# Performance work log

Hardware: AMD Instinct MI355X
Metric: run time of the kernel (lower is better)

The kernel has to match this reference:

```python
import jax, jax.numpy as jnp
import numpy as np

B, N, L = 16, 512, 512          # batch, compound atoms, protein words
DIM = 10                         # compound feature dim
DM, H, DK, DFF = 128, 8, 16, 512 # transformer dims
LG, LO = 3, 3                    # layer_gnn, layer_output
NFP, NW = 10000, 10000           # vocab sizes
NEG = -9e15                      # GAT mask sentinel (matches torch code)


def _layernorm(x, g, b, eps=1e-6):
    # annotated-transformer LayerNorm: unbiased std, eps added to std
    m = jnp.mean(x, -1, keepdims=True)
    s = jnp.std(x, -1, keepdims=True, ddof=1)
    return g * (x - m) / (s + eps) + b


def _pos_encoding(length, d_model):
    pos = np.arange(length)[:, None]
    div = np.exp(np.arange(0, d_model, 2) * (-np.log(10000.0) / d_model))
    pe = np.zeros((length, d_model), np.float32)
    pe[:, 0::2] = np.sin(pos * div)
    pe[:, 1::2] = np.cos(pos * div)
    return jnp.asarray(pe)


def setup_inputs():
    ks = iter(jax.random.split(jax.random.key(0), 64))
    def nrm(shape, scale):
        return jax.random.normal(next(ks), shape, jnp.float32) * scale
    return dict(
        fingerprints=jax.random.randint(next(ks), (B, N), 0, NFP, jnp.int32),
        fp_mask=jnp.ones((B, N), jnp.float32),
        adjacency=jax.random.randint(next(ks), (B, N, N), 0, 2, jnp.int32),
        words=jax.random.randint(next(ks), (B, L), 0, NW, jnp.int32),
        words_mask=jnp.ones((B, L), jnp.float32),
        emb_fp=nrm((NFP, DIM), 0.1),
        emb_word=nrm((NW, DM), 0.1),
        Wg=nrm((LG, DIM, DIM), 0.3), bg=jnp.zeros((LG, DIM), jnp.float32),
        attn_a=nrm((LG, 2 * DIM), 0.3),
        Wq=nrm((DM, DM), 0.09), bq=jnp.zeros((DM,), jnp.float32),
        Wk=nrm((DM, DM), 0.09), bk=jnp.zeros((DM,), jnp.float32),
        Wv=nrm((DM, DM), 0.09), bv=jnp.zeros((DM,), jnp.float32),
        Wo=nrm((DM, DM), 0.09), bo=jnp.zeros((DM,), jnp.float32),
        ln1_g=jnp.ones((DM,), jnp.float32), ln1_b=jnp.zeros((DM,), jnp.float32),
        ln2_g=jnp.ones((DM,), jnp.float32), ln2_b=jnp.zeros((DM,), jnp.float32),
        lnf_g=jnp.ones((DM,), jnp.float32), lnf_b=jnp.zeros((DM,), jnp.float32),
        W1=nrm((DM, DFF), 0.09), b1=jnp.zeros((DFF,), jnp.float32),
        W2=nrm((DFF, DM), 0.045), b2=jnp.zeros((DM,), jnp.float32),
        Wtout=nrm((DM, DIM), 0.09), btout=jnp.zeros((DIM,), jnp.float32),
        Watt=nrm((DIM, DIM), 0.3), batt=jnp.zeros((DIM,), jnp.float32),
        Wout=nrm((LO, 2 * DIM, 2 * DIM), 0.2), bout=jnp.zeros((LO, 2 * DIM), jnp.float32),
        Wint=nrm((2 * DIM, 2), 0.2), bint=jnp.zeros((2,), jnp.float32),
    )


def _forward(fingerprints, fp_mask, adjacency, words, words_mask,
             emb_fp, emb_word, Wg, bg, attn_a,
             Wq, bq, Wk, bk, Wv, bv, Wo, bo,
             ln1_g, ln1_b, ln2_g, ln2_b, lnf_g, lnf_b,
             W1, b1, W2, b2, Wtout, btout,
             Watt, batt, Wout, bout, Wint, bint):
    # ---- GAT over compound graph (dropout disabled = eval/deterministic) ----
    xs = emb_fp[fingerprints]                     # [B,N,DIM]
    mask = fp_mask[:, :, None]                    # [B,N,1]
    adj = adjacency > 0
    for i in range(LG):
        h = jax.nn.relu(xs @ Wg[i] + bg[i]) * mask
        # e[b,i,j] = leaky_relu(a1.h_i + a2.h_j)  == leaky_relu([h_i||h_j] @ a)
        s1 = h @ attn_a[i, :DIM]                  # [B,N]
        s2 = h @ attn_a[i, DIM:]                  # [B,N]
        e = jax.nn.leaky_relu(s1[:, :, None] + s2[:, None, :])  # [B,N,N]
        att = jax.nn.softmax(jnp.where(adj, e, NEG), axis=2)
        xs = xs + att @ h
    compound = jnp.mean(xs * mask, axis=1, keepdims=True)       # [B,1,DIM]

    # ---- transformer encoder, 1 layer, annotated-transformer (pre-norm) ----
    x = emb_word[words] * jnp.sqrt(jnp.float32(DM)) + _pos_encoding(L, DM)
    m4 = words_mask[:, None, None, :] > 0         # [B,1,1,L]
    xn = _layernorm(x, ln1_g, ln1_b)
    heads = lambda t: t.reshape(B, L, H, DK).transpose(0, 2, 1, 3)
    q, k, v = heads(xn @ Wq + bq), heads(xn @ Wk + bk), heads(xn @ Wv + bv)
    scores = jnp.einsum('bhqd,bhkd->bhqk', q, k) / jnp.sqrt(jnp.float32(DK))
    p = jax.nn.softmax(jnp.where(m4, scores, -1e9), axis=-1)
    attn = jnp.einsum('bhqk,bhkd->bhqd', p, v).transpose(0, 2, 1, 3).reshape(B, L, DM)
    x = x + (attn @ Wo + bo)
    xn = _layernorm(x, ln2_g, ln2_b)
    x = x + (jax.nn.relu(xn @ W1 + b1) @ W2 + b2)
    x = _layernorm(x, lnf_g, lnf_b)
    word_vectors = jax.nn.relu(x) @ Wtout + btout  # [B,L,DIM]

    # ---- tanh cross-attention (attention_cnn) ----
    hc = jax.nn.relu(compound @ Watt + batt)       # [B,1,DIM]
    hp = jax.nn.relu(word_vectors @ Watt + batt)   # [B,L,DIM]
    w = jnp.tanh(jnp.einsum('bxd,bld->bxl', hc, hp))  # [B,1,L]
    protein = jnp.mean(w.transpose(0, 2, 1) * hp, axis=1, keepdims=True)  # [B,1,DIM]

    cat = jnp.concatenate([compound, protein], axis=2)  # [B,1,2*DIM]
    for j in range(LO):
        cat = jax.nn.relu(cat @ Wout[j] + bout[j])
    return jnp.squeeze(cat @ Wint + bint, axis=1)        # [B,2]


def reference(fingerprints, fp_mask, adjacency, words, words_mask,
              emb_fp, emb_word, Wg, bg, attn_a,
              Wq, bq, Wk, bk, Wv, bv, Wo, bo,
              ln1_g, ln1_b, ln2_g, ln2_b, lnf_g, lnf_b,
              W1, b1, W2, b2, Wtout, btout,
              Watt, batt, Wout, bout, Wint, bint):
    return _forward(fingerprints, fp_mask, adjacency, words, words_mask,
                    emb_fp, emb_word, Wg, bg, attn_a,
                    Wq, bq, Wk, bk, Wv, bv, Wo, bo,
                    ln1_g, ln1_b, ln2_g, ln2_b, lnf_g, lnf_b,
                    W1, b1, W2, b2, Wtout, btout,
                    Watt, batt, Wout, bout, Wint, bint)
```

## Files before the change

### kernel.cpp

```cpp
#include <hip/hip_runtime.h>
#include <hip/hip_bf16.h>
#include <math.h>

#define B 16
#define N 512
#define L 512
#define DIM 10
#define DM 128
#define H 8
#define DK 16
#define DFF 512
#define LG 3
#define LO 3
#define NEGV -9.0e15f
#define RF 16
#define AQR 64

__device__ __forceinline__ float wave_reduce_sum(float v) {
    #pragma unroll
    for (int o = 32; o > 0; o >>= 1) v += __shfl_down(v, o, 64);
    return v;
}


__global__ void k_embed_fp(const int* __restrict__ fing, const float* __restrict__ emb_fp,
                           float* __restrict__ xs) {
    int idx = blockIdx.x * blockDim.x + threadIdx.x;
    if (idx >= B * N * DIM) return;
    int d = idx % DIM;
    int bn = idx / DIM;
    xs[idx] = emb_fp[fing[bn] * DIM + d];
}

__global__ void k_gnn_h(const float* __restrict__ xs, const float* __restrict__ fp_mask,
                        const float* __restrict__ Wg, const float* __restrict__ bg,
                        const float* __restrict__ aatt,
                        float* __restrict__ h, float* __restrict__ s1, float* __restrict__ s2) {
    int bn = blockIdx.x * blockDim.x + threadIdx.x;
    if (bn >= B * N) return;
    float x[DIM];
    #pragma unroll
    for (int d = 0; d < DIM; d++) x[d] = xs[bn * DIM + d];
    float m = fp_mask[bn];
    float a1 = 0.f, a2 = 0.f;
    #pragma unroll
    for (int j = 0; j < DIM; j++) {
        float acc = bg[j];
        #pragma unroll
        for (int d = 0; d < DIM; d++) acc += x[d] * Wg[d * DIM + j];
        acc = fmaxf(acc, 0.f) * m;
        h[bn * DIM + j] = acc;
        a1 += acc * aatt[j];
        a2 += acc * aatt[DIM + j];
    }
    s1[bn] = a1;
    s2[bn] = a2;
}

__global__ void k_gnn_att(const float* __restrict__ h, const float* __restrict__ s1,
                          const float* __restrict__ s2, const int* __restrict__ adj,
                          float* __restrict__ xs) {
    int b  = blockIdx.x / (N / 16);
    int rg = blockIdx.x % (N / 16);
    int t = threadIdx.x;
    int g  = t >> 4;
    int ll = t & 15;
    int i = rg * 16 + g;

    __shared__ float h_s[N * DIM];
    __shared__ float s2_s[N];

    const float* hb = h + (long)b * N * DIM;
    for (int idx = t; idx < N * DIM; idx += 256) h_s[idx] = hb[idx];
    for (int j = t; j < N; j += 256) s2_s[j] = s2[b * N + j];
    __syncthreads();

    float s1v = s1[b * N + i];
    const int* adjrow = adj + ((long)b * N + i) * N;

    float e[32];
    #pragma unroll
    for (int c = 0; c < 32; c++) {
        int j = c * 16 + ll;
        float xsc = s1v + s2_s[j];
        xsc = xsc > 0.f ? xsc : 0.01f * xsc;
        e[c] = (adjrow[j] > 0) ? xsc : NEGV;
    }
    float m = e[0];
    #pragma unroll
    for (int c = 1; c < 32; c++) m = fmaxf(m, e[c]);
    #pragma unroll
    for (int off = 1; off < 16; off <<= 1) m = fmaxf(m, __shfl_xor(m, off, 64));

    float sum = 0.f;
    float a[DIM];
    #pragma unroll
    for (int d = 0; d < DIM; d++) a[d] = 0.f;
    #pragma unroll
    for (int c = 0; c < 32; c++) {
        float p = expf(e[c] - m);
        sum += p;
        int j = c * 16 + ll;
        #pragma unroll
        for (int d = 0; d < DIM; d++) a[d] += p * h_s[j * DIM + d];
    }
    #pragma unroll
    for (int off = 1; off < 16; off <<= 1) {
        sum += __shfl_xor(sum, off, 64);
        #pragma unroll
        for (int d = 0; d < DIM; d++) a[d] += __shfl_xor(a[d], off, 64);
    }
    if (ll < DIM) {
        float av = a[0];
        if (ll == 1) av = a[1]; else if (ll == 2) av = a[2]; else if (ll == 3) av = a[3];
        else if (ll == 4) av = a[4]; else if (ll == 5) av = a[5]; else if (ll == 6) av = a[6];
        else if (ll == 7) av = a[7]; else if (ll == 8) av = a[8]; else if (ll == 9) av = a[9];
        xs[((long)b * N + i) * DIM + ll] += av / sum;
    }
}

__global__ void k_compound(const float* __restrict__ xs, const float* __restrict__ fp_mask,
                           const float* __restrict__ Watt, const float* __restrict__ batt,
                           float* __restrict__ compound, float* __restrict__ hc) {
    int b = blockIdx.x;
    int t = threadIdx.x;
    int wid = t >> 6, lane = t & 63;
    float lacc[DIM];
    #pragma unroll
    for (int d = 0; d < DIM; d++) lacc[d] = 0.f;
    for (int n = t; n < N; n += 256) {
        float m = fp_mask[b * N + n];
        #pragma unroll
        for (int d = 0; d < DIM; d++) lacc[d] += xs[((long)b * N + n) * DIM + d] * m;
    }
    __shared__ float red[4][DIM];
    __shared__ float comp_s[DIM];
    #pragma unroll
    for (int d = 0; d < DIM; d++) lacc[d] = wave_reduce_sum(lacc[d]);
    if (lane == 0) {
        #pragma unroll
        for (int d = 0; d < DIM; d++) red[wid][d] = lacc[d];
    }
    __syncthreads();
    if (t < DIM) {
        float c = (red[0][t] + red[1][t] + red[2][t] + red[3][t]) / (float)N;
        compound[b * DIM + t] = c;
        comp_s[t] = c;
    }
    __syncthreads();
    if (t < DIM) {
        float acc = batt[t];
        #pragma unroll
        for (int e = 0; e < DIM; e++) acc += comp_s[e] * Watt[e * DIM + t];
        hc[b * DIM + t] = fmaxf(acc, 0.f);
    }
}


__global__ void k_pe(float* __restrict__ pe) {
    int idx = blockIdx.x * blockDim.x + threadIdx.x;
    if (idx >= L * DM) return;
    int d = idx % DM, l = idx / DM;
    int k = d >> 1;
    double div = exp((double)(2 * k) * (-log(10000.0) / (double)DM));
    double ang = (double)l * div;
    pe[idx] = (d & 1) ? (float)cos(ang) : (float)sin(ang);
}

__global__ void k_embed_word(const int* __restrict__ words, const float* __restrict__ emb,
                             const float* __restrict__ pe, float* __restrict__ x) {
    long idx = (long)blockIdx.x * blockDim.x + threadIdx.x;
    if (idx >= (long)B * L * DM) return;
    int d = idx % DM;
    long bl = idx / DM;
    int l = (int)(bl % L);
    x[idx] = emb[(long)words[bl] * DM + d] * sqrtf(128.0f) + pe[l * DM + d];
}

__global__ void k_layernorm(const float* __restrict__ x, const float* __restrict__ g,
                            const float* __restrict__ bb, float* __restrict__ out) {
    int row = blockIdx.x;
    int t = threadIdx.x;
    int wid = t >> 6, lane = t & 63;
    float v = x[(long)row * DM + t];
    float s = wave_reduce_sum(v);
    __shared__ float r2[2], r3[2];
    if (lane == 0) r2[wid] = s;
    __syncthreads();
    float mean = (r2[0] + r2[1]) / (float)DM;
    float dv = v - mean;
    float q = wave_reduce_sum(dv * dv);
    if (lane == 0) r3[wid] = q;
    __syncthreads();
    float sd = sqrtf((r3[0] + r3[1]) / (float)(DM - 1)) + 1e-6f;
    out[(long)row * DM + t] = g[t] * dv / sd + bb[t];
}

__global__ void k_qkv(const float* __restrict__ xn,
                      const float* __restrict__ Wq, const float* __restrict__ bq,
                      const float* __restrict__ Wk, const float* __restrict__ bk,
                      const float* __restrict__ Wv, const float* __restrict__ bv,
                      float* __restrict__ q, float* __restrict__ k, float* __restrict__ v) {
    long row0 = (long)blockIdx.x * RF;
    int t = threadIdx.x;
    __shared__ float xs_s[RF * DM];
    for (int i = t; i < RF * DM; i += 384) xs_s[i] = xn[row0 * DM + i];
    __syncthreads();
    int proj = t / DM;
    int j = t % DM;
    const float* W    = proj == 0 ? Wq : (proj == 1 ? Wk : Wv);
    const float* bias = proj == 0 ? bq : (proj == 1 ? bk : bv);
    float* out        = proj == 0 ? q  : (proj == 1 ? k  : v);
    float acc[RF];
    #pragma unroll
    for (int r = 0; r < RF; r++) acc[r] = bias[j];
    for (int d = 0; d < DM; d++) {
        float w = W[d * DM + j];
        #pragma unroll
        for (int r = 0; r < RF; r++) acc[r] += xs_s[r * DM + d] * w;
    }
    #pragma unroll
    for (int r = 0; r < RF; r++) {
        long row = row0 + r;
        int b = (int)(row / L), l = (int)(row % L);
        out[(((long)b * H + j / DK) * L + l) * DK + (j % DK)] = acc[r];
    }
}

__global__ void k_attn(const float* __restrict__ q, const float* __restrict__ k,
                       const float* __restrict__ v, const float* __restrict__ wmask,
                       float* __restrict__ attnout) {
    int blk = blockIdx.x;
    int qc = blk % (L / AQR);
    int bh = blk / (L / AQR);
    int b = bh / H, hh = bh % H;
    int t = threadIdx.x;
    int sl = t & 3;
    int r = t >> 2;
    int l = qc * AQR + r;

    __shared__ float4 k_s[L * 4];
    __shared__ float wm_s[L];
    const float4* kb4 = (const float4*)(k + (long)bh * L * DK);
    for (int i = t; i < L * 4; i += 256) k_s[i] = kb4[i];
    for (int j = t; j < L; j += 256) wm_s[j] = wmask[b * L + j];
    __syncthreads();

    float4 qr = ((const float4*)(q + ((long)bh * L + l) * DK))[sl];
    qr.x *= 0.25f; qr.y *= 0.25f; qr.z *= 0.25f; qr.w *= 0.25f;

    const float4* vb4 = (const float4*)(v + (long)bh * L * DK);

    float m = -1e30f, ssum = 0.f;
    float4 acc = make_float4(0.f, 0.f, 0.f, 0.f);

    for (int c = 0; c < L / 8; c++) {
        int j0 = c * 8;
        float s8[8];
        #pragma unroll
        for (int jj = 0; jj < 8; jj++) {
            float4 kk = k_s[(j0 + jj) * 4 + sl];
            s8[jj] = qr.x * kk.x + qr.y * kk.y + qr.z * kk.z + qr.w * kk.w;
        }
        #pragma unroll
        for (int jj = 0; jj < 8; jj++) {
            s8[jj] += __shfl_xor(s8[jj], 1, 64);
            s8[jj] += __shfl_xor(s8[jj], 2, 64);
            s8[jj] = (wm_s[j0 + jj] > 0.f) ? s8[jj] : -1e9f;
        }
        float cm = fmaxf(fmaxf(fmaxf(s8[0], s8[1]), fmaxf(s8[2], s8[3])),
                         fmaxf(fmaxf(s8[4], s8[5]), fmaxf(s8[6], s8[7])));
        float mn = fmaxf(m, cm);
        float scale = __expf(m - mn);
        ssum *= scale;
        acc.x *= scale; acc.y *= scale; acc.z *= scale; acc.w *= scale;
        #pragma unroll
        for (int jj = 0; jj < 8; jj++) {
            float p = __expf(s8[jj] - mn);
            ssum += p;
            float4 vv = vb4[(j0 + jj) * 4 + sl];
            acc.x += p * vv.x; acc.y += p * vv.y; acc.z += p * vv.z; acc.w += p * vv.w;
        }
        m = mn;
    }

    float inv = 1.f / ssum;
    float4* outp = (float4*)(attnout + ((long)b * L + l) * DM + hh * DK);
    outp[sl] = make_float4(acc.x * inv, acc.y * inv, acc.z * inv, acc.w * inv);
}

__global__ void k_oproj(const float* __restrict__ attnout, const float* __restrict__ Wo,
                        const float* __restrict__ bo, float* __restrict__ x) {
    long row0 = (long)blockIdx.x * RF;
    int t = threadIdx.x;
    __shared__ float a_s[RF * DM];
    for (int i = t; i < RF * DM; i += 128) a_s[i] = attnout[row0 * DM + i];
    __syncthreads();
    float acc[RF];
    #pragma unroll
    for (int r = 0; r < RF; r++) acc[r] = bo[t];
    for (int d = 0; d < DM; d++) {
        float w = Wo[d * DM + t];
        #pragma unroll
        for (int r = 0; r < RF; r++) acc[r] += a_s[r * DM + d] * w;
    }
    #pragma unroll
    for (int r = 0; r < RF; r++) x[(row0 + r) * DM + t] += acc[r];
}

__global__ void k_ffn(const float* __restrict__ xn, const float* __restrict__ W1,
                      const float* __restrict__ b1, const float* __restrict__ W2,
                      const float* __restrict__ b2, float* __restrict__ x) {
    long row0 = (long)blockIdx.x * RF;
    int t = threadIdx.x;
    __shared__ float xs_s[RF * DM];
    __shared__ float h_s[RF * DFF];
    for (int i = t; i < RF * DM; i += 512) xs_s[i] = xn[row0 * DM + i];
    __syncthreads();
    {
        float acc[RF];
        #pragma unroll
        for (int r = 0; r < RF; r++) acc[r] = b1[t];
        for (int d = 0; d < DM; d++) {
            float w = W1[d * DFF + t];
            #pragma unroll
            for (int r = 0; r < RF; r++) acc[r] += xs_s[r * DM + d] * w;
        }
        #pragma unroll
        for (int r = 0; r < RF; r++) h_s[r * DFF + t] = fmaxf(acc[r], 0.f);
    }
    __syncthreads();
    int col = t & 127, rq = t >> 7;
    float acc2[4];
    #pragma unroll
    for (int rr = 0; rr < 4; rr++) acc2[rr] = b2[col];
    for (int f = 0; f < DFF; f++) {
        float w = W2[f * DM + col];
        #pragma unroll
        for (int rr = 0; rr < 4; rr++) acc2[rr] += h_s[(rq * 4 + rr) * DFF + f] * w;
    }
    #pragma unroll
    for (int rr = 0; rr < 4; rr++) x[(row0 + rq * 4 + rr) * DM + col] += acc2[rr];
}

__global__ void k_lnf_hp(const float* __restrict__ x, const float* __restrict__ g,
                         const float* __restrict__ bb, const float* __restrict__ Wtout,
                         const float* __restrict__ btout, const float* __restrict__ Watt,
                         const float* __restrict__ batt, float* __restrict__ hp) {
    int row = blockIdx.x;
    int t = threadIdx.x;
    int wid = t >> 6, lane = t & 63;
    float v = x[(long)row * DM + t];
    float s = wave_reduce_sum(v);
    __shared__ float r2[2], r3[2];
    if (lane == 0) r2[wid] = s;
    __syncthreads();
    float mean = (r2[0] + r2[1]) / (float)DM;
    float dv = v - mean;
    float qq = wave_reduce_sum(dv * dv);
    if (lane == 0) r3[wid] = qq;
    __syncthreads();
    float sd = sqrtf((r3[0] + r3[1]) / (float)(DM - 1)) + 1e-6f;
    float xnv = g[t] * dv / sd + bb[t];
    __shared__ float rrelu[DM];
    rrelu[t] = fmaxf(xnv, 0.f);
    __syncthreads();
    __shared__ float wv_s[DIM];
    if (t < DIM) {
        float acc = btout[t];
        for (int d = 0; d < DM; d++) acc += rrelu[d] * Wtout[d * DIM + t];
        wv_s[t] = acc;
    }
    __syncthreads();
    if (t < DIM) {
        float acc = batt[t];
        #pragma unroll
        for (int e = 0; e < DIM; e++) acc += wv_s[e] * Watt[e * DIM + t];
        hp[(long)row * DIM + t] = fmaxf(acc, 0.f);
    }
}

__global__ void k_final(const float* __restrict__ hp, const float* __restrict__ hc,
                        const float* __restrict__ compound, const float* __restrict__ Wout,
                        const float* __restrict__ bout, const float* __restrict__ Wint,
                        const float* __restrict__ bint, float* __restrict__ out) {
    int b = blockIdx.x;
    int t = threadIdx.x;
    int wid = t >> 6, lane = t & 63;

    __shared__ float wout_s[LO * 2 * DIM * 2 * DIM];
    __shared__ float bout_s[LO * 2 * DIM];
    __shared__ float wint_s[2 * DIM * 2];
    __shared__ float bint_s[2];
    __shared__ float hc_s[DIM];
    __shared__ float red[4][DIM];
    __shared__ float cat_s[2 * DIM];
    __shared__ float tmp_s[2 * DIM];

    for (int i = t; i < LO * 2 * DIM * 2 * DIM; i += 256) wout_s[i] = Wout[i];
    for (int i = t; i < LO * 2 * DIM; i += 256) bout_s[i] = bout[i];
    for (int i = t; i < 2 * DIM * 2; i += 256) wint_s[i] = Wint[i];
    if (t < 2) bint_s[t] = bint[t];
    if (t < DIM) hc_s[t] = hc[b * DIM + t];
    __syncthreads();

    float lacc[DIM];
    #pragma unroll
    for (int e = 0; e < DIM; e++) lacc[e] = 0.f;
    for (int l = t; l < L; l += 256) {
        const float* hpl = hp + ((long)b * L + l) * DIM;
        float hv[DIM];
        float dot = 0.f;
        #pragma unroll
        for (int e = 0; e < DIM; e++) { hv[e] = hpl[e]; dot += hc_s[e] * hv[e]; }
        float w = tanhf(dot);
        #pragma unroll
        for (int e = 0; e < DIM; e++) lacc[e] += w * hv[e];
    }
    #pragma unroll
    for (int e = 0; e < DIM; e++) lacc[e] = wave_reduce_sum(lacc[e]);
    if (lane == 0) {
        #pragma unroll
        for (int e = 0; e < DIM; e++) red[wid][e] = lacc[e];
    }
    __syncthreads();
    if (t < DIM) {
        cat_s[t] = compound[b * DIM + t];
        cat_s[DIM + t] = (red[0][t] + red[1][t] + red[2][t] + red[3][t]) / (float)L;
    }
    __syncthreads();

    for (int j = 0; j < LO; j++) {
        float acc = 0.f;
        if (t < 2 * DIM) {
            acc = bout_s[j * 2 * DIM + t];
            #pragma unroll
            for (int e = 0; e < 2 * DIM; e++)
                acc += cat_s[e] * wout_s[j * 2 * DIM * 2 * DIM + e * 2 * DIM + t];
            acc = fmaxf(acc, 0.f);
            tmp_s[t] = acc;
        }
        __syncthreads();
        if (t < 2 * DIM) cat_s[t] = tmp_s[t];
        __syncthreads();
    }
    if (t < 2) {
        float o = bint_s[t];
        #pragma unroll
        for (int e = 0; e < 2 * DIM; e++) o += cat_s[e] * wint_s[e * 2 + t];
        out[b * 2 + t] = o;
    }
}

extern "C" void kernel_launch(void* const* d_in, const int* in_sizes, int n_in,
                              void* d_out, int out_size, void* d_ws, size_t ws_size,
                              hipStream_t stream) {
    (void)in_sizes; (void)n_in; (void)out_size; (void)ws_size;
    const int*   fingerprints = (const int*)d_in[0];
    const float* fp_mask      = (const float*)d_in[1];
    const int*   adjacency    = (const int*)d_in[2];
    const int*   words        = (const int*)d_in[3];
    const float* words_mask   = (const float*)d_in[4];
    const float* emb_fp       = (const float*)d_in[5];
    const float* emb_word     = (const float*)d_in[6];
    const float* Wg   = (const float*)d_in[7];
    const float* bg   = (const float*)d_in[8];
    const float* attn_a = (const float*)d_in[9];
    const float* Wq = (const float*)d_in[10];
    const float* bq = (const float*)d_in[11];
    const float* Wk = (const float*)d_in[12];
    const float* bk = (const float*)d_in[13];
    const float* Wv = (const float*)d_in[14];
    const float* bv = (const float*)d_in[15];
    const float* Wo = (const float*)d_in[16];
    const float* bo = (const float*)d_in[17];
    const float* ln1_g = (const float*)d_in[18];
    const float* ln1_b = (const float*)d_in[19];
    const float* ln2_g = (const float*)d_in[20];
    const float* ln2_b = (const float*)d_in[21];
    const float* lnf_g = (const float*)d_in[22];
    const float* lnf_b = (const float*)d_in[23];
    const float* W1 = (const float*)d_in[24];
    const float* b1 = (const float*)d_in[25];
    const float* W2 = (const float*)d_in[26];
    const float* b2 = (const float*)d_in[27];
    const float* Wtout = (const float*)d_in[28];
    const float* btout = (const float*)d_in[29];
    const float* Watt  = (const float*)d_in[30];
    const float* batt  = (const float*)d_in[31];
    const float* Wout  = (const float*)d_in[32];
    const float* bout  = (const float*)d_in[33];
    const float* Wint  = (const float*)d_in[34];
    const float* bint  = (const float*)d_in[35];
    float* out = (float*)d_out;

    float* w = (float*)d_ws;
    float* xs = w;        w += B * N * DIM;
    float* h  = w;        w += B * N * DIM;
    float* s1 = w;        w += B * N;
    float* s2 = w;        w += B * N;
    float* compound = w;  w += B * DIM;
    float* hc = w;        w += B * DIM;
    float* pe = w;        w += L * DM;
    float* x  = w;        w += (long)B * L * DM;
    float* xn = w;        w += (long)B * L * DM;
    float* qb = w;        w += (long)B * H * L * DK;
    float* kb = w;        w += (long)B * H * L * DK;
    float* vb = w;        w += (long)B * H * L * DK;
    float* attnout = w;   w += (long)B * L * DM;
    float* hp = w;        w += (long)B * L * DIM;

    k_embed_fp<<<(B * N * DIM + 255) / 256, 256, 0, stream>>>(fingerprints, emb_fp, xs);
    for (int i = 0; i < LG; i++) {
        k_gnn_h<<<(B * N + 255) / 256, 256, 0, stream>>>(
            xs, fp_mask, Wg + i * DIM * DIM, bg + i * DIM, attn_a + i * 2 * DIM, h, s1, s2);
        k_gnn_att<<<B * (N / 16), 256, 0, stream>>>(h, s1, s2, adjacency, xs);
    }
    k_compound<<<B, 256, 0, stream>>>(xs, fp_mask, Watt, batt, compound, hc);

    k_pe<<<(L * DM + 255) / 256, 256, 0, stream>>>(pe);
    k_embed_word<<<(B * L * DM + 255) / 256, 256, 0, stream>>>(words, emb_word, pe, x);
    k_layernorm<<<B * L, DM, 0, stream>>>(x, ln1_g, ln1_b, xn);
    k_qkv<<<B * L / RF, 3 * DM, 0, stream>>>(xn, Wq, bq, Wk, bk, Wv, bv, qb, kb, vb);
    k_attn<<<B * H * (L / AQR), 256, 0, stream>>>(qb, kb, vb, words_mask, attnout);
    k_oproj<<<B * L / RF, DM, 0, stream>>>(attnout, Wo, bo, x);
    k_layernorm<<<B * L, DM, 0, stream>>>(x, ln2_g, ln2_b, xn);
    k_ffn<<<B * L / RF, DFF, 0, stream>>>(xn, W1, b1, W2, b2, x);
    k_lnf_hp<<<B * L, DM, 0, stream>>>(x, lnf_g, lnf_b, Wtout, btout, Watt, batt, hp);
    k_final<<<B, 256, 0, stream>>>(hp, hc, compound, Wout, bout, Wint, bint, out);
}
```

Measured before the change: 277.1 us.

## Restructure attention kernel into split-key flash attention with two queries per thread

Each thread now computes two query rows across the full 16-dim head over one eighth of the key range, instead of four threads sharing a row's dimensions and scanning all keys. K, V and the mask are read directly from global memory rather than staged in shared memory, and the eight partial softmax states are merged with xor shuffles at the end. This removes the per-score cross-lane reductions and the shared-memory staging barrier, and reuses each K/V load across two queries. In exchange it uses many more registers, reads K/V through the cache instead of LDS, and adds a log-step merge epilogue.

```diff
diff --git a/kernel.cpp b/kernel.cpp
--- a/kernel.cpp
+++ b/kernel.cpp
@@ -235,58 +235,122 @@
     int bh = blk / (L / AQR);
     int b = bh / H, hh = bh % H;
     int t = threadIdx.x;
-    int sl = t & 3;
-    int r = t >> 2;
-    int l = qc * AQR + r;
-
-    __shared__ float4 k_s[L * 4];
-    __shared__ float wm_s[L];
+    int seg = t & 7;
+    int pr = t >> 3;
+    int l0 = qc * AQR + pr * 2;
+
+    const float4* qp = (const float4*)(q + ((long)bh * L + l0) * DK);
+    float4 qa0 = qp[0], qa1 = qp[1], qa2 = qp[2], qa3 = qp[3];
+    float4 qb0 = qp[4], qb1 = qp[5], qb2 = qp[6], qb3 = qp[7];
+    qa0.x*=0.25f;qa0.y*=0.25f;qa0.z*=0.25f;qa0.w*=0.25f;
+    qa1.x*=0.25f;qa1.y*=0.25f;qa1.z*=0.25f;qa1.w*=0.25f;
+    qa2.x*=0.25f;qa2.y*=0.25f;qa2.z*=0.25f;qa2.w*=0.25f;
+    qa3.x*=0.25f;qa3.y*=0.25f;qa3.z*=0.25f;qa3.w*=0.25f;
+    qb0.x*=0.25f;qb0.y*=0.25f;qb0.z*=0.25f;qb0.w*=0.25f;
+    qb1.x*=0.25f;qb1.y*=0.25f;qb1.z*=0.25f;qb1.w*=0.25f;
+    qb2.x*=0.25f;qb2.y*=0.25f;qb2.z*=0.25f;qb2.w*=0.25f;
+    qb3.x*=0.25f;qb3.y*=0.25f;qb3.z*=0.25f;qb3.w*=0.25f;
+
     const float4* kb4 = (const float4*)(k + (long)bh * L * DK);
-    for (int i = t; i < L * 4; i += 256) k_s[i] = kb4[i];
-    for (int j = t; j < L; j += 256) wm_s[j] = wmask[b * L + j];
-    __syncthreads();
-
-    float4 qr = ((const float4*)(q + ((long)bh * L + l) * DK))[sl];
-    qr.x *= 0.25f; qr.y *= 0.25f; qr.z *= 0.25f; qr.w *= 0.25f;
-
     const float4* vb4 = (const float4*)(v + (long)bh * L * DK);
-
-    float m = -1e30f, ssum = 0.f;
-    float4 acc = make_float4(0.f, 0.f, 0.f, 0.f);
-
-    for (int c = 0; c < L / 8; c++) {
-        int j0 = c * 8;
-        float s8[8];
+    const float4* wm4 = (const float4*)(wmask + (long)b * L);
+
+    float m0 = -1e30f, m1 = -1e30f, ss0 = 0.f, ss1 = 0.f;
+    float4 a00 = make_float4(0,0,0,0), a01 = a00, a02 = a00, a03 = a00;
+    float4 a10 = a00, a11 = a00, a12 = a00, a13 = a00;
+
+    for (int c = 0; c < 8; c++) {
+        int j0 = seg * 64 + c * 8;
+        float s0[8], s1[8];
         #pragma unroll
         for (int jj = 0; jj < 8; jj++) {
-            float4 kk = k_s[(j0 + jj) * 4 + sl];
-            s8[jj] = qr.x * kk.x + qr.y * kk.y + qr.z * kk.z + qr.w * kk.w;
+            const float4* kp = kb4 + (long)(j0 + jj) * 4;
+            float4 k0 = kp[0], k1 = kp[1], k2 = kp[2], k3 = kp[3];
+            s0[jj] = qa0.x*k0.x + qa0.y*k0.y + qa0.z*k0.z + qa0.w*k0.w
+                   + qa1.x*k1.x + qa1.y*k1.y + qa1.z*k1.z + qa1.w*k1.w
+                   + qa2.x*k2.x + qa2.y*k2.y + qa2.z*k2.z + qa2.w*k2.w
+                   + qa3.x*k3.x + qa3.y*k3.y + qa3.z*k3.z + qa3.w*k3.w;
+            s1[jj] = qb0.x*k0.x + qb0.y*k0.y + qb0.z*k0.z + qb0.w*k0.w
+                   + qb1.x*k1.x + qb1.y*k1.y + qb1.z*k1.z + qb1.w*k1.w
+                   + qb2.x*k2.x + qb2.y*k2.y + qb2.z*k2.z + qb2.w*k2.w
+                   + qb3.x*k3.x + qb3.y*k3.y + qb3.z*k3.z + qb3.w*k3.w;
         }
+        float4 wma = wm4[j0 / 4], wmb = wm4[j0 / 4 + 1];
+        s0[0] = wma.x > 0.f ? s0[0] : -1e9f;  s1[0] = wma.x > 0.f ? s1[0] : -1e9f;
+        s0[1] = wma.y > 0.f ? s0[1] : -1e9f;  s1[1] = wma.y > 0.f ? s1[1] : -1e9f;
+        s0[2] = wma.z > 0.f ? s0[2] : -1e9f;  s1[2] = wma.z > 0.f ? s1[2] : -1e9f;
+        s0[3] = wma.w > 0.f ? s0[3] : -1e9f;  s1[3] = wma.w > 0.f ? s1[3] : -1e9f;
+        s0[4] = wmb.x > 0.f ? s0[4] : -1e9f;  s1[4] = wmb.x > 0.f ? s1[4] : -1e9f;
+        s0[5] = wmb.y > 0.f ? s0[5] : -1e9f;  s1[5] = wmb.y > 0.f ? s1[5] : -1e9f;
+        s0[6] = wmb.z > 0.f ? s0[6] : -1e9f;  s1[6] = wmb.z > 0.f ? s1[6] : -1e9f;
+        s0[7] = wmb.w > 0.f ? s0[7] : -1e9f;  s1[7] = wmb.w > 0.f ? s1[7] : -1e9f;
+
+        float cm0 = fmaxf(fmaxf(fmaxf(s0[0],s0[1]),fmaxf(s0[2],s0[3])),
+                          fmaxf(fmaxf(s0[4],s0[5]),fmaxf(s0[6],s0[7])));
+        float cm1 = fmaxf(fmaxf(fmaxf(s1[0],s1[1]),fmaxf(s1[2],s1[3])),
+                          fmaxf(fmaxf(s1[4],s1[5]),fmaxf(s1[6],s1[7])));
+        float mn0 = fmaxf(m0, cm0), mn1 = fmaxf(m1, cm1);
+        float sc0 = __expf(m0 - mn0), sc1 = __expf(m1 - mn1);
+        ss0 *= sc0; ss1 *= sc1;
+        a00.x*=sc0;a00.y*=sc0;a00.z*=sc0;a00.w*=sc0;
+        a01.x*=sc0;a01.y*=sc0;a01.z*=sc0;a01.w*=sc0;
+        a02.x*=sc0;a02.y*=sc0;a02.z*=sc0;a02.w*=sc0;
+        a03.x*=sc0;a03.y*=sc0;a03.z*=sc0;a03.w*=sc0;
+        a10.x*=sc1;a10.y*=sc1;a10.z*=sc1;a10.w*=sc1;
+        a11.x*=sc1;a11.y*=sc1;a11.z*=sc1;a11.w*=sc1;
+        a12.x*=sc1;a12.y*=sc1;a12.z*=sc1;a12.w*=sc1;
+        a13.x*=sc1;a13.y*=sc1;a13.z*=sc1;a13.w*=sc1;
+        m0 = mn0; m1 = mn1;
+
         #pragma unroll
         for (int jj = 0; jj < 8; jj++) {
-            s8[jj] += __shfl_xor(s8[jj], 1, 64);
-            s8[jj] += __shfl_xor(s8[jj], 2, 64);
-            s8[jj] = (wm_s[j0 + jj] > 0.f) ? s8[jj] : -1e9f;
+            float p0 = __expf(s0[jj] - m0);
+            float p1 = __expf(s1[jj] - m1);
+            ss0 += p0; ss1 += p1;
+            const float4* vp = vb4 + (long)(j0 + jj) * 4;
+            float4 v0 = vp[0], v1 = vp[1], v2 = vp[2], v3 = vp[3];
+            a00.x += p0*v0.x; a00.y += p0*v0.y; a00.z += p0*v0.z; a00.w += p0*v0.w;
+            a01.x += p0*v1.x; a01.y += p0*v1.y; a01.z += p0*v1.z; a01.w += p0*v1.w;
+            a02.x += p0*v2.x; a02.y += p0*v2.y; a02.z += p0*v2.z; a02.w += p0*v2.w;
+            a03.x += p0*v3.x; a03.y += p0*v3.y; a03.z += p0*v3.z; a03.w += p0*v3.w;
+            a10.x += p1*v0.x; a10.y += p1*v0.y; a10.z += p1*v0.z; a10.w += p1*v0.w;
+            a11.x += p1*v1.x; a11.y += p1*v1.y; a11.z += p1*v1.z; a11.w += p1*v1.w;
+            a12.x += p1*v2.x; a12.y += p1*v2.y; a12.z += p1*v2.z; a12.w += p1*v2.w;
+            a13.x += p1*v3.x; a13.y += p1*v3.y; a13.z += p1*v3.z; a13.w += p1*v3.w;
         }
-        float cm = fmaxf(fmaxf(fmaxf(s8[0], s8[1]), fmaxf(s8[2], s8[3])),
-                         fmaxf(fmaxf(s8[4], s8[5]), fmaxf(s8[6], s8[7])));
-        float mn = fmaxf(m, cm);
-        float scale = __expf(m - mn);
-        ssum *= scale;
-        acc.x *= scale; acc.y *= scale; acc.z *= scale; acc.w *= scale;
-        #pragma unroll
-        for (int jj = 0; jj < 8; jj++) {
-            float p = __expf(s8[jj] - mn);
-            ssum += p;
-            float4 vv = vb4[(j0 + jj) * 4 + sl];
-            acc.x += p * vv.x; acc.y += p * vv.y; acc.z += p * vv.z; acc.w += p * vv.w;
-        }
-        m = mn;
-    }
-
-    float inv = 1.f / ssum;
-    float4* outp = (float4*)(attnout + ((long)b * L + l) * DM + hh * DK);
-    outp[sl] = make_float4(acc.x * inv, acc.y * inv, acc.z * inv, acc.w * inv);
+    }
+
+    #pragma unroll
+    for (int off = 1; off <= 4; off <<= 1) {
+        float m0o = __shfl_xor(m0, off, 64), m1o = __shfl_xor(m1, off, 64);
+        float s0o = __shfl_xor(ss0, off, 64), s1o = __shfl_xor(ss1, off, 64);
+        float mn0 = fmaxf(m0, m0o), mn1 = fmaxf(m1, m1o);
+        float ea0 = __expf(m0 - mn0), eb0 = __expf(m0o - mn0);
+        float ea1 = __expf(m1 - mn1), eb1 = __expf(m1o - mn1);
+        ss0 = ss0 * ea0 + s0o * eb0;
+        ss1 = ss1 * ea1 + s1o * eb1;
+        #define MRG0(f) { float o_ = __shfl_xor(f, off, 64); f = f * ea0 + o_ * eb0; }
+        #define MRG1(f) { float o_ = __shfl_xor(f, off, 64); f = f * ea1 + o_ * eb1; }
+        MRG0(a00.x) MRG0(a00.y) MRG0(a00.z) MRG0(a00.w)
+        MRG0(a01.x) MRG0(a01.y) MRG0(a01.z) MRG0(a01.w)
+        MRG0(a02.x) MRG0(a02.y) MRG0(a02.z) MRG0(a02.w)
+        MRG0(a03.x) MRG0(a03.y) MRG0(a03.z) MRG0(a03.w)
+        MRG1(a10.x) MRG1(a10.y) MRG1(a10.z) MRG1(a10.w)
+        MRG1(a11.x) MRG1(a11.y) MRG1(a11.z) MRG1(a11.w)
+        MRG1(a12.x) MRG1(a12.y) MRG1(a12.z) MRG1(a12.w)
+        MRG1(a13.x) MRG1(a13.y) MRG1(a13.z) MRG1(a13.w)
+        #undef MRG0
+        #undef MRG1
+        m0 = mn0; m1 = mn1;
+    }
+
+    int sl = seg & 3, rr = seg >> 2;
+    float inv = 1.f / (rr ? ss1 : ss0);
+    float4 w4;
+    if (rr == 0) w4 = (sl == 0) ? a00 : (sl == 1) ? a01 : (sl == 2) ? a02 : a03;
+    else         w4 = (sl == 0) ? a10 : (sl == 1) ? a11 : (sl == 2) ? a12 : a13;
+    float4* outp = (float4*)(attnout + ((long)b * L + (l0 + rr)) * DM + hh * DK);
+    outp[sl] = make_float4(w4.x * inv, w4.y * inv, w4.z * inv, w4.w * inv);
 }
 
 __global__ void k_oproj(const float* __restrict__ attnout, const float* __restrict__ Wo,
```

Result: slower. 467.6 us (+68.7%).

## Split attention keys across waves with per-lane full-row queries and merge partials

Applied to the files above, without the earlier changes.

The attention kernel now gives each lane a whole query row and splits the key range across the four waves, one quarter each. K and V are read straight from global memory as wave-uniform broadcast loads, which removes the shared-memory K staging and the shuffle reduction over head-dim sub-lanes. The per-wave online-softmax partials are combined through shared memory by wave 0. This increases register use per thread (16-element accumulators) and adds a merge step, and launch bounds are set to keep occupancy.

```diff
diff --git a/kernel.cpp b/kernel.cpp
--- a/kernel.cpp
+++ b/kernel.cpp
@@ -227,66 +227,113 @@
     }
 }
 
-__global__ void k_attn(const float* __restrict__ q, const float* __restrict__ k,
-                       const float* __restrict__ v, const float* __restrict__ wmask,
-                       float* __restrict__ attnout) {
+__global__ void __launch_bounds__(256, 4)
+k_attn(const float* __restrict__ q, const float* __restrict__ k,
+       const float* __restrict__ v, const float* __restrict__ wmask,
+       float* __restrict__ attnout) {
     int blk = blockIdx.x;
     int qc = blk % (L / AQR);
     int bh = blk / (L / AQR);
     int b = bh / H, hh = bh % H;
     int t = threadIdx.x;
-    int sl = t & 3;
-    int r = t >> 2;
-    int l = qc * AQR + r;
-
-    __shared__ float4 k_s[L * 4];
-    __shared__ float wm_s[L];
+    int lane = t & 63;
+    int wv = t >> 6;
+    int l = qc * AQR + lane;
+
+    const float4* qp = (const float4*)(q + ((long)bh * L + l) * DK);
+    float4 q0 = qp[0], q1 = qp[1], q2 = qp[2], q3 = qp[3];
+    q0.x*=0.25f;q0.y*=0.25f;q0.z*=0.25f;q0.w*=0.25f;
+    q1.x*=0.25f;q1.y*=0.25f;q1.z*=0.25f;q1.w*=0.25f;
+    q2.x*=0.25f;q2.y*=0.25f;q2.z*=0.25f;q2.w*=0.25f;
+    q3.x*=0.25f;q3.y*=0.25f;q3.z*=0.25f;q3.w*=0.25f;
+
     const float4* kb4 = (const float4*)(k + (long)bh * L * DK);
-    for (int i = t; i < L * 4; i += 256) k_s[i] = kb4[i];
-    for (int j = t; j < L; j += 256) wm_s[j] = wmask[b * L + j];
-    __syncthreads();
-
-    float4 qr = ((const float4*)(q + ((long)bh * L + l) * DK))[sl];
-    qr.x *= 0.25f; qr.y *= 0.25f; qr.z *= 0.25f; qr.w *= 0.25f;
-
     const float4* vb4 = (const float4*)(v + (long)bh * L * DK);
-
-    float m = -1e30f, ssum = 0.f;
-    float4 acc = make_float4(0.f, 0.f, 0.f, 0.f);
-
-    for (int c = 0; c < L / 8; c++) {
-        int j0 = c * 8;
+    const float4* wm4 = (const float4*)(wmask + (long)b * L);
+
+    float m = -1e30f, ss = 0.f;
+    float4 a0 = make_float4(0,0,0,0), a1 = a0, a2 = a0, a3 = a0;
+
+    for (int c = 0; c < 16; c++) {
+        int j0 = wv * 128 + c * 8;
         float s8[8];
         #pragma unroll
         for (int jj = 0; jj < 8; jj++) {
-            float4 kk = k_s[(j0 + jj) * 4 + sl];
-            s8[jj] = qr.x * kk.x + qr.y * kk.y + qr.z * kk.z + qr.w * kk.w;
+            const float4* kp = kb4 + (long)(j0 + jj) * 4;
+            float4 k0 = kp[0], k1 = kp[1], k2 = kp[2], k3 = kp[3];
+            s8[jj] = q0.x*k0.x + q0.y*k0.y + q0.z*k0.z + q0.w*k0.w
+                   + q1.x*k1.x + q1.y*k1.y + q1.z*k1.z + q1.w*k1.w
+                   + q2.x*k2.x + q2.y*k2.y + q2.z*k2.z + q2.w*k2.w
+                   + q3.x*k3.x + q3.y*k3.y + q3.z*k3.z + q3.w*k3.w;
         }
+        float4 wma = wm4[j0 / 4], wmb = wm4[j0 / 4 + 1];
+        s8[0] = wma.x > 0.f ? s8[0] : -1e9f;
+        s8[1] = wma.y > 0.f ? s8[1] : -1e9f;
+        s8[2] = wma.z > 0.f ? s8[2] : -1e9f;
+        s8[3] = wma.w > 0.f ? s8[3] : -1e9f;
+        s8[4] = wmb.x > 0.f ? s8[4] : -1e9f;
+        s8[5] = wmb.y > 0.f ? s8[5] : -1e9f;
+        s8[6] = wmb.z > 0.f ? s8[6] : -1e9f;
+        s8[7] = wmb.w > 0.f ? s8[7] : -1e9f;
+
+        float cm = fmaxf(fmaxf(fmaxf(s8[0],s8[1]),fmaxf(s8[2],s8[3])),
+                         fmaxf(fmaxf(s8[4],s8[5]),fmaxf(s8[6],s8[7])));
+        float mn = fmaxf(m, cm);
+        float sc = __expf(m - mn);
+        ss *= sc;
+        a0.x*=sc;a0.y*=sc;a0.z*=sc;a0.w*=sc;
+        a1.x*=sc;a1.y*=sc;a1.z*=sc;a1.w*=sc;
+        a2.x*=sc;a2.y*=sc;a2.z*=sc;a2.w*=sc;
+        a3.x*=sc;a3.y*=sc;a3.z*=sc;a3.w*=sc;
+        m = mn;
+
         #pragma unroll
         for (int jj = 0; jj < 8; jj++) {
-            s8[jj] += __shfl_xor(s8[jj], 1, 64);
-            s8[jj] += __shfl_xor(s8[jj], 2, 64);
-            s8[jj] = (wm_s[j0 + jj] > 0.f) ? s8[jj] : -1e9f;
+            float p = __expf(s8[jj] - m);
+            ss += p;
+            const float4* vp = vb4 + (long)(j0 + jj) * 4;
+            float4 v0 = vp[0], v1 = vp[1], v2 = vp[2], v3 = vp[3];
+            a0.x += p*v0.x; a0.y += p*v0.y; a0.z += p*v0.z; a0.w += p*v0.w;
+            a1.x += p*v1.x; a1.y += p*v1.y; a1.z += p*v1.z; a1.w += p*v1.w;
+            a2.x += p*v2.x; a2.y += p*v2.y; a2.z += p*v2.z; a2.w += p*v2.w;
+            a3.x += p*v3.x; a3.y += p*v3.y; a3.z += p*v3.z; a3.w += p*v3.w;
         }
-        float cm = fmaxf(fmaxf(fmaxf(s8[0], s8[1]), fmaxf(s8[2], s8[3])),
-                         fmaxf(fmaxf(s8[4], s8[5]), fmaxf(s8[6], s8[7])));
-        float mn = fmaxf(m, cm);
-        float scale = __expf(m - mn);
-        ssum *= scale;
-        acc.x *= scale; acc.y *= scale; acc.z *= scale; acc.w *= scale;
-        #pragma unroll
-        for (int jj = 0; jj < 8; jj++) {
-            float p = __expf(s8[jj] - mn);
-            ssum += p;
-            float4 vv = vb4[(j0 + jj) * 4 + sl];
-            acc.x += p * vv.x; acc.y += p * vv.y; acc.z += p * vv.z; acc.w += p * vv.w;
+    }
+
+    __shared__ float part[3][AQR][18];
+    if (wv > 0) {
+        float* p_ = &part[wv - 1][lane][0];
+        p_[0] = m;    p_[1] = ss;
+        p_[2] = a0.x; p_[3] = a0.y; p_[4]  = a0.z; p_[5]  = a0.w;
+        p_[6] = a1.x; p_[7] = a1.y; p_[8]  = a1.z; p_[9]  = a1.w;
+        p_[10]= a2.x; p_[11]= a2.y; p_[12] = a2.z; p_[13] = a2.w;
+        p_[14]= a3.x; p_[15]= a3.y; p_[16] = a3.z; p_[17] = a3.w;
+    }
+    __syncthreads();
+    if (wv == 0) {
+        for (int s = 0; s < 3; s++) {
+            const float* p_ = &part[s][lane][0];
+            float m2 = p_[0], ss2 = p_[1];
+            float mn = fmaxf(m, m2);
+            float ea = __expf(m - mn), eb = __expf(m2 - mn);
+            ss = ss * ea + ss2 * eb;
+            a0.x = a0.x*ea + p_[2]*eb;  a0.y = a0.y*ea + p_[3]*eb;
+            a0.z = a0.z*ea + p_[4]*eb;  a0.w = a0.w*ea + p_[5]*eb;
+            a1.x = a1.x*ea + p_[6]*eb;  a1.y = a1.y*ea + p_[7]*eb;
+            a1.z = a1.z*ea + p_[8]*eb;  a1.w = a1.w*ea + p_[9]*eb;
+            a2.x = a2.x*ea + p_[10]*eb; a2.y = a2.y*ea + p_[11]*eb;
+            a2.z = a2.z*ea + p_[12]*eb; a2.w = a2.w*ea + p_[13]*eb;
+            a3.x = a3.x*ea + p_[14]*eb; a3.y = a3.y*ea + p_[15]*eb;
+            a3.z = a3.z*ea + p_[16]*eb; a3.w = a3.w*ea + p_[17]*eb;
+            m = mn;
         }
-        m = mn;
-    }
-
-    float inv = 1.f / ssum;
-    float4* outp = (float4*)(attnout + ((long)b * L + l) * DM + hh * DK);
-    outp[sl] = make_float4(acc.x * inv, acc.y * inv, acc.z * inv, acc.w * inv);
+        float inv = 1.f / ss;
+        float4* outp = (float4*)(attnout + ((long)b * L + l) * DM + hh * DK);
+        outp[0] = make_float4(a0.x*inv, a0.y*inv, a0.z*inv, a0.w*inv);
+        outp[1] = make_float4(a1.x*inv, a1.y*inv, a1.z*inv, a1.w*inv);
+        outp[2] = make_float4(a2.x*inv, a2.y*inv, a2.z*inv, a2.w*inv);
+        outp[3] = make_float4(a3.x*inv, a3.y*inv, a3.z*inv, a3.w*inv);
+    }
 }
 
 __global__ void k_oproj(const float* __restrict__ attnout, const float* __restrict__ Wo,
```

Measured after the change: 305.0 us. 10.1% more time.

## Restructure attention kernel with double-buffered K/V tiles and key-split per thread

Applied to the files above, without the earlier changes.

The attention kernel now streams K, V and the mask through double-buffered 64-key shared-memory tiles, with a swizzled layout to avoid bank conflicts. Previously only K sat in shared memory and V was read directly from global memory. Each thread now computes two query rows over a slice of 8 keys, so every K/V shared load is reused across both rows. The eight key-groups are merged with shuffle reductions at the end. This is meant to cut per-key global V traffic and shuffle overhead, at the cost of more registers and a barrier on every tile.

```diff
diff --git a/kernel.cpp b/kernel.cpp
--- a/kernel.cpp
+++ b/kernel.cpp
@@ -15,11 +15,21 @@
 #define NEGV -9.0e15f
 #define RF 16
 #define AQR 64
+#define KT 64
+#define NT (L / KT)
 
 __device__ __forceinline__ float wave_reduce_sum(float v) {
     #pragma unroll
     for (int o = 32; o > 0; o >>= 1) v += __shfl_down(v, o, 64);
     return v;
+}
+
+__device__ __forceinline__ float dot16(float4 q0, float4 q1, float4 q2, float4 q3,
+                                       float4 k0, float4 k1, float4 k2, float4 k3) {
+    return q0.x*k0.x + q0.y*k0.y + q0.z*k0.z + q0.w*k0.w
+         + q1.x*k1.x + q1.y*k1.y + q1.z*k1.z + q1.w*k1.w
+         + q2.x*k2.x + q2.y*k2.y + q2.z*k2.z + q2.w*k2.w
+         + q3.x*k3.x + q3.y*k3.y + q3.z*k3.z + q3.w*k3.w;
 }
 
 
@@ -227,66 +237,163 @@
     }
 }
 
-__global__ void k_attn(const float* __restrict__ q, const float* __restrict__ k,
-                       const float* __restrict__ v, const float* __restrict__ wmask,
-                       float* __restrict__ attnout) {
+__global__ void __launch_bounds__(256, 4)
+k_attn(const float* __restrict__ q, const float* __restrict__ k,
+       const float* __restrict__ v, const float* __restrict__ wmask,
+       float* __restrict__ attnout) {
     int blk = blockIdx.x;
     int qc = blk % (L / AQR);
     int bh = blk / (L / AQR);
     int b = bh / H, hh = bh % H;
     int t = threadIdx.x;
-    int sl = t & 3;
-    int r = t >> 2;
-    int l = qc * AQR + r;
-
-    __shared__ float4 k_s[L * 4];
-    __shared__ float wm_s[L];
+    int qg = t >> 3;
+    int kg = t & 7;
+
+    __shared__ float kbuf[2][KT][DK];
+    __shared__ float vbuf[2][KT][DK];
+    __shared__ float mbuf[2][KT];
+
     const float4* kb4 = (const float4*)(k + (long)bh * L * DK);
-    for (int i = t; i < L * 4; i += 256) k_s[i] = kb4[i];
-    for (int j = t; j < L; j += 256) wm_s[j] = wmask[b * L + j];
-    __syncthreads();
-
-    float4 qr = ((const float4*)(q + ((long)bh * L + l) * DK))[sl];
-    qr.x *= 0.25f; qr.y *= 0.25f; qr.z *= 0.25f; qr.w *= 0.25f;
-
     const float4* vb4 = (const float4*)(v + (long)bh * L * DK);
-
-    float m = -1e30f, ssum = 0.f;
-    float4 acc = make_float4(0.f, 0.f, 0.f, 0.f);
-
-    for (int c = 0; c < L / 8; c++) {
-        int j0 = c * 8;
-        float s8[8];
-        #pragma unroll
-        for (int jj = 0; jj < 8; jj++) {
-            float4 kk = k_s[(j0 + jj) * 4 + sl];
-            s8[jj] = qr.x * kk.x + qr.y * kk.y + qr.z * kk.z + qr.w * kk.w;
-        }
-        #pragma unroll
-        for (int jj = 0; jj < 8; jj++) {
-            s8[jj] += __shfl_xor(s8[jj], 1, 64);
-            s8[jj] += __shfl_xor(s8[jj], 2, 64);
-            s8[jj] = (wm_s[j0 + jj] > 0.f) ? s8[jj] : -1e9f;
-        }
-        float cm = fmaxf(fmaxf(fmaxf(s8[0], s8[1]), fmaxf(s8[2], s8[3])),
-                         fmaxf(fmaxf(s8[4], s8[5]), fmaxf(s8[6], s8[7])));
-        float mn = fmaxf(m, cm);
-        float scale = __expf(m - mn);
-        ssum *= scale;
-        acc.x *= scale; acc.y *= scale; acc.z *= scale; acc.w *= scale;
-        #pragma unroll
-        for (int jj = 0; jj < 8; jj++) {
-            float p = __expf(s8[jj] - mn);
-            ssum += p;
-            float4 vv = vb4[(j0 + jj) * 4 + sl];
-            acc.x += p * vv.x; acc.y += p * vv.y; acc.z += p * vv.z; acc.w += p * vv.w;
-        }
-        m = mn;
-    }
-
-    float inv = 1.f / ssum;
-    float4* outp = (float4*)(attnout + ((long)b * L + l) * DM + hh * DK);
-    outp[sl] = make_float4(acc.x * inv, acc.y * inv, acc.z * inv, acc.w * inv);
+    const float*  wm  = wmask + (long)b * L;
+
+    int row0 = qc * AQR + 2 * qg;
+    const float4* qp = (const float4*)(q + ((long)bh * L + row0) * DK);
+    float4 qa[4], qb[4];
+    #pragma unroll
+    for (int i = 0; i < 4; i++) {
+        qa[i] = qp[i];     qb[i] = qp[4 + i];
+        qa[i].x *= 0.25f; qa[i].y *= 0.25f; qa[i].z *= 0.25f; qa[i].w *= 0.25f;
+        qb[i].x *= 0.25f; qb[i].y *= 0.25f; qb[i].z *= 0.25f; qb[i].w *= 0.25f;
+    }
+
+    int skey = t >> 2;
+    int spart = t & 3;
+    int sphys = spart ^ ((skey >> 3) & 3);
+
+    {
+        float4 kr = kb4[t];
+        float4 vr = vb4[t];
+        ((float4*)&kbuf[0][skey][0])[sphys] = kr;
+        ((float4*)&vbuf[0][skey][0])[sphys] = vr;
+        if (t < KT) mbuf[0][t] = (wm[t] > 0.f) ? 0.f : -1e9f;
+    }
+    __syncthreads();
+
+    float m0 = -1e30f, m1 = -1e30f, ss0 = 0.f, ss1 = 0.f;
+    float4 o0[4], o1[4];
+    #pragma unroll
+    for (int i = 0; i < 4; i++) {
+        o0[i] = make_float4(0.f, 0.f, 0.f, 0.f);
+        o1[i] = make_float4(0.f, 0.f, 0.f, 0.f);
+    }
+
+    int sw = kg & 3;
+    int cur = 0;
+    for (int tt = 0; tt < NT; tt++) {
+        float4 kr2, vr2;
+        float mr2 = 1.f;
+        if (tt < NT - 1) {
+            long base = (long)(tt + 1) * KT * 4;
+            kr2 = kb4[base + t];
+            vr2 = vb4[base + t];
+            if (t < KT) mr2 = wm[(tt + 1) * KT + t];
+        }
+
+        float s0[8], s1[8];
+        #pragma unroll
+        for (int kk = 0; kk < 8; kk++) {
+            const float4* kp = (const float4*)&kbuf[cur][kg * 8 + kk][0];
+            float4 k0 = kp[0 ^ sw], k1 = kp[1 ^ sw], k2 = kp[2 ^ sw], k3 = kp[3 ^ sw];
+            s0[kk] = dot16(qa[0], qa[1], qa[2], qa[3], k0, k1, k2, k3);
+            s1[kk] = dot16(qb[0], qb[1], qb[2], qb[3], k0, k1, k2, k3);
+        }
+        {
+            const float4* mp = (const float4*)&mbuf[cur][kg * 8];
+            float4 ma = mp[0], mb_ = mp[1];
+            s0[0] += ma.x;  s1[0] += ma.x;   s0[1] += ma.y;  s1[1] += ma.y;
+            s0[2] += ma.z;  s1[2] += ma.z;   s0[3] += ma.w;  s1[3] += ma.w;
+            s0[4] += mb_.x; s1[4] += mb_.x;  s0[5] += mb_.y; s1[5] += mb_.y;
+            s0[6] += mb_.z; s1[6] += mb_.z;  s0[7] += mb_.w; s1[7] += mb_.w;
+        }
+
+        float cm0 = fmaxf(fmaxf(fmaxf(s0[0], s0[1]), fmaxf(s0[2], s0[3])),
+                          fmaxf(fmaxf(s0[4], s0[5]), fmaxf(s0[6], s0[7])));
+        float cm1 = fmaxf(fmaxf(fmaxf(s1[0], s1[1]), fmaxf(s1[2], s1[3])),
+                          fmaxf(fmaxf(s1[4], s1[5]), fmaxf(s1[6], s1[7])));
+        cm0 = fmaxf(cm0, __shfl_xor(cm0, 1, 64));
+        cm0 = fmaxf(cm0, __shfl_xor(cm0, 2, 64));
+        cm0 = fmaxf(cm0, __shfl_xor(cm0, 4, 64));
+        cm1 = fmaxf(cm1, __shfl_xor(cm1, 1, 64));
+        cm1 = fmaxf(cm1, __shfl_xor(cm1, 2, 64));
+        cm1 = fmaxf(cm1, __shfl_xor(cm1, 4, 64));
+
+        float mn0 = fmaxf(m0, cm0), mn1 = fmaxf(m1, cm1);
+        float sc0 = __expf(m0 - mn0), sc1 = __expf(m1 - mn1);
+        m0 = mn0; m1 = mn1;
+
+        float pls0 = 0.f, pls1 = 0.f;
+        #pragma unroll
+        for (int kk = 0; kk < 8; kk++) {
+            s0[kk] = __expf(s0[kk] - mn0); pls0 += s0[kk];
+            s1[kk] = __expf(s1[kk] - mn1); pls1 += s1[kk];
+        }
+        ss0 = ss0 * sc0 + pls0;
+        ss1 = ss1 * sc1 + pls1;
+        #pragma unroll
+        for (int i = 0; i < 4; i++) {
+            o0[i].x *= sc0; o0[i].y *= sc0; o0[i].z *= sc0; o0[i].w *= sc0;
+            o1[i].x *= sc1; o1[i].y *= sc1; o1[i].z *= sc1; o1[i].w *= sc1;
+        }
+
+        #pragma unroll
+        for (int kk = 0; kk < 8; kk++) {
+            const float4* vp = (const float4*)&vbuf[cur][kg * 8 + kk][0];
+            float4 v0 = vp[0 ^ sw], v1 = vp[1 ^ sw], v2 = vp[2 ^ sw], v3 = vp[3 ^ sw];
+            float p0 = s0[kk], p1 = s1[kk];
+            o0[0].x += p0*v0.x; o0[0].y += p0*v0.y; o0[0].z += p0*v0.z; o0[0].w += p0*v0.w;
+            o0[1].x += p0*v1.x; o0[1].y += p0*v1.y; o0[1].z += p0*v1.z; o0[1].w += p0*v1.w;
+            o0[2].x += p0*v2.x; o0[2].y += p0*v2.y; o0[2].z += p0*v2.z; o0[2].w += p0*v2.w;
+            o0[3].x += p0*v3.x; o0[3].y += p0*v3.y; o0[3].z += p0*v3.z; o0[3].w += p0*v3.w;
+            o1[0].x += p1*v0.x; o1[0].y += p1*v0.y; o1[0].z += p1*v0.z; o1[0].w += p1*v0.w;
+            o1[1].x += p1*v1.x; o1[1].y += p1*v1.y; o1[1].z += p1*v1.z; o1[1].w += p1*v1.w;
+            o1[2].x += p1*v2.x; o1[2].y += p1*v2.y; o1[2].z += p1*v2.z; o1[2].w += p1*v2.w;
+            o1[3].x += p1*v3.x; o1[3].y += p1*v3.y; o1[3].z += p1*v3.z; o1[3].w += p1*v3.w;
+        }
+
+        if (tt < NT - 1) {
+            ((float4*)&kbuf[cur ^ 1][skey][0])[sphys] = kr2;
+            ((float4*)&vbuf[cur ^ 1][skey][0])[sphys] = vr2;
+            if (t < KT) mbuf[cur ^ 1][t] = (mr2 > 0.f) ? 0.f : -1e9f;
+        }
+        __syncthreads();
+        cur ^= 1;
+    }
+
+    #pragma unroll
+    for (int off = 1; off <= 4; off <<= 1) {
+        ss0 += __shfl_xor(ss0, off, 64);
+        ss1 += __shfl_xor(ss1, off, 64);
+        #pragma unroll
+        for (int i = 0; i < 4; i++) {
+            o0[i].x += __shfl_xor(o0[i].x, off, 64);
+            o0[i].y += __shfl_xor(o0[i].y, off, 64);
+            o0[i].z += __shfl_xor(o0[i].z, off, 64);
+            o0[i].w += __shfl_xor(o0[i].w, off, 64);
+            o1[i].x += __shfl_xor(o1[i].x, off, 64);
+            o1[i].y += __shfl_xor(o1[i].y, off, 64);
+            o1[i].z += __shfl_xor(o1[i].z, off, 64);
+            o1[i].w += __shfl_xor(o1[i].w, off, 64);
+        }
+    }
+
+    int rsel = kg >> 2, qsel = kg & 3;
+    float4 t0 = (qsel == 0) ? o0[0] : (qsel == 1) ? o0[1] : (qsel == 2) ? o0[2] : o0[3];
+    float4 t1 = (qsel == 0) ? o1[0] : (qsel == 1) ? o1[1] : (qsel == 2) ? o1[2] : o1[3];
+    float4 ov = rsel ? t1 : t0;
+    float inv = 1.f / (rsel ? ss1 : ss0);
+    float4* outp = (float4*)(attnout + ((long)b * L + (row0 + rsel)) * DM + hh * DK);
+    outp[qsel] = make_float4(ov.x * inv, ov.y * inv, ov.z * inv, ov.w * inv);
 }
 
 __global__ void k_oproj(const float* __restrict__ attnout, const float* __restrict__ Wo,
```

Result: slower. 313.1 us (+13.0%).
